# Performance work log

Hardware: AMD Instinct MI355X
Metric: run time of the kernel (lower is better)

The kernel has to match this reference:

```python
import jax, jax.numpy as jnp
import numpy as np

N, E = 50000, 800000
IN_DIM, HID, H1, H2, NCLS = 512, 64, 4, 1, 40
NEG_SLOPE = 0.2


def gat_conv(x, src, dst, W, att_src, att_dst, b, heads, ch):
    # x: [N, F_in]; W: [F_in, heads*ch]; att_*: [heads, ch]; b: [heads*ch]
    n = x.shape[0]
    h = (x @ W).reshape(n, heads, ch)                      # [N,H,C]
    a_s = jnp.einsum('nhc,hc->nh', h, att_src)             # [N,H]
    a_d = jnp.einsum('nhc,hc->nh', h, att_dst)             # [N,H]
    e = jax.nn.leaky_relu(a_s[src] + a_d[dst], NEG_SLOPE)  # [E,H]
    # segment softmax over incoming edges of each destination node
    m = jax.ops.segment_max(e, dst, num_segments=n)        # [N,H]
    ex = jnp.exp(e - m[dst])
    s = jax.ops.segment_sum(ex, dst, num_segments=n)       # [N,H]
    alpha = ex / (s[dst] + 1e-16)                          # [E,H]
    out = jax.ops.segment_sum(alpha[:, :, None] * h[src], dst, num_segments=n)
    return out.reshape(n, heads * ch) + b


def setup_inputs() -> dict:
    key = jax.random.key(0)
    ks = jax.random.split(key, 10)
    glorot = lambda k, shp: jax.random.normal(k, shp, jnp.float32) * jnp.sqrt(2.0 / (shp[0] + shp[-1]))
    return {
        'x': jax.random.normal(ks[0], (N, IN_DIM), jnp.float32),
        'edge_index': jax.random.randint(ks[1], (2, E), 0, N, jnp.int64),
        'W1': glorot(ks[2], (IN_DIM, H1 * HID)),
        'att_src1': glorot(ks[3], (H1, HID)),
        'att_dst1': glorot(ks[4], (H1, HID)),
        'b1': jnp.zeros((H1 * HID,), jnp.float32),
        'W2': glorot(ks[5], (H1 * HID, H2 * NCLS)),
        'att_src2': glorot(ks[6], (H2, NCLS)),
        'att_dst2': glorot(ks[7], (H2, NCLS)),
        'b2': jnp.zeros((H2 * NCLS,), jnp.float32),
    }


def reference(x, edge_index, W1, att_src1, att_dst1, b1, W2, att_src2, att_dst2, b2):
    n = x.shape[0]
    loops = jnp.arange(n, dtype=edge_index.dtype)
    src = jnp.concatenate([edge_index[0], loops])  # add self loops (PyG default)
    dst = jnp.concatenate([edge_index[1], loops])
    # dropout layers are identity in eval mode
    h = gat_conv(x, src, dst, W1, att_src1, att_dst1, b1, H1, HID)
    h = jax.nn.elu(h)
    out = gat_conv(h, src, dst, W2, att_src2, att_dst2, b2, H2, NCLS)
    return jax.nn.log_softmax(out, axis=1)
```

## Files before the change

### kernel.cpp

```cpp
#include <hip/hip_runtime.h>
#include <math.h>
#include <stdint.h>


typedef short bf16x8 __attribute__((ext_vector_type(8)));
typedef float f32x4  __attribute__((ext_vector_type(4)));

static __device__ __forceinline__ float leaky(float x){ return x > 0.f ? x : 0.2f*x; }
static __device__ __forceinline__ unsigned short f2bf(float f){
  uint32_t u = __float_as_uint(f);
  uint32_t r = u + 0x7fffu + ((u >> 16) & 1u);
  return (unsigned short)(r >> 16);
}
static __device__ __forceinline__ float bf2f(unsigned short u){
  return __uint_as_float(((uint32_t)u) << 16);
}

__global__ void k_cvt_x(const float* __restrict__ x, unsigned short* __restrict__ xb, int n4){
  int i = blockIdx.x*blockDim.x + threadIdx.x;
  if (i >= n4) return;
  float4 v = ((const float4*)x)[i];
  ushort4 o; o.x=f2bf(v.x); o.y=f2bf(v.y); o.z=f2bf(v.z); o.w=f2bf(v.w);
  ((ushort4*)xb)[i] = o;
}

__global__ void k_cvt_w(const float* __restrict__ W, unsigned short* __restrict__ wt){
  int i = blockIdx.x*blockDim.x + threadIdx.x;
  if (i >= 512*256) return;
  int k = i >> 8, n = i & 255;
  wt[n*512 + k] = f2bf(W[i]);
}

__global__ void k_count(const int* __restrict__ ei, int E, int n, int* __restrict__ deg){
  int i = blockIdx.x*blockDim.x + threadIdx.x;
  int tot = E + n;
  if (i >= tot) return;
  int dst = (i < E) ? ei[E + i] : (i - E);
  atomicAdd(&deg[dst], 1);
}

__global__ __launch_bounds__(256) void k_scan_a(const int* __restrict__ deg,
    int* __restrict__ rowstart, int* __restrict__ bsum, int n){
  __shared__ int sm[256];
  int b = blockIdx.x, t = threadIdx.x;
  int i = b*256 + t;
  int v = (i < n) ? deg[i] : 0;
  sm[t] = v;
  __syncthreads();
  for (int off=1; off<256; off<<=1){
    int u = (t >= off) ? sm[t-off] : 0;
    __syncthreads();
    sm[t] += u;
    __syncthreads();
  }
  if (i < n) rowstart[i+1] = sm[t];
  if (t == 255) bsum[b] = sm[255];
}
__global__ __launch_bounds__(256) void k_scan_b(int* __restrict__ bsum, int nb){
  __shared__ int sm[256];
  int t = threadIdx.x;
  int v = (t < nb) ? bsum[t] : 0;
  sm[t] = v;
  __syncthreads();
  for (int off=1; off<256; off<<=1){
    int u = (t >= off) ? sm[t-off] : 0;
    __syncthreads();
    sm[t] += u;
    __syncthreads();
  }
  if (t < nb) bsum[t] = sm[t] - v;
}
__global__ __launch_bounds__(256) void k_scan_c(int* __restrict__ rowstart,
    const int* __restrict__ bsum, int n){
  int b = blockIdx.x, t = threadIdx.x;
  int i = b*256 + t;
  if (i < n) rowstart[i+1] += bsum[b];
  if (i == 0) rowstart[0] = 0;
}

__global__ void k_fill(const int* __restrict__ ei, int E, int n,
                       const int* __restrict__ rowstart, int* __restrict__ cur, int* __restrict__ csr){
  int i = blockIdx.x*blockDim.x + threadIdx.x;
  int tot = E + n;
  if (i >= tot) return;
  int src, dst;
  if (i < E){ src = ei[i]; dst = ei[E+i]; } else { src = i - E; dst = src; }
  int pos = atomicAdd(&cur[dst], 1);
  csr[rowstart[dst] + pos] = src;
}

__global__ __launch_bounds__(256) void k_gemm1_mfma(const unsigned short* __restrict__ A,
                                                    const unsigned short* __restrict__ BT,
                                                    const float* __restrict__ SW,
                                                    const float* __restrict__ DW,
                                                    unsigned short* __restrict__ Cb,
                                                    float* __restrict__ as1,
                                                    float* __restrict__ ad1, int M){
  __shared__ __align__(16) unsigned short lA[4*128*8];
  __shared__ __align__(16) unsigned short lB[4*128*8];
  const int t = threadIdx.x;
  const int lane = t & 63, w = t >> 6;
  const int wx = w & 1, wy = w >> 1;
  const int row0 = blockIdx.x * 128, col0 = blockIdx.y * 128;

  f32x4 acc[4][4];
  #pragma unroll
  for (int i=0;i<4;i++)
    #pragma unroll
    for (int j=0;j<4;j++)
      #pragma unroll
      for (int r=0;r<4;r++) acc[i][j][r] = 0.f;

  const int c0 = t, c1 = t + 256;
  const int r0 = c0 & 127, kq0 = c0 >> 7;
  const int r1 = c1 & 127, kq1 = c1 >> 7;
  const size_t gA0 = (size_t)min(row0 + r0, M-1)*512 + kq0*8;
  const size_t gA1 = (size_t)min(row0 + r1, M-1)*512 + kq1*8;
  const size_t gB0 = (size_t)(col0 + r0)*512 + kq0*8;
  const size_t gB1 = (size_t)(col0 + r1)*512 + kq1*8;

  const int kq = lane >> 4, li = lane & 15;

  for (int kt = 0; kt < 512; kt += 32){
    __builtin_amdgcn_global_load_lds((const __attribute__((address_space(1))) void*)(A + gA0 + kt),
        (__attribute__((address_space(3))) void*)&lA[c0*8], 16, 0, 0);
    __builtin_amdgcn_global_load_lds((const __attribute__((address_space(1))) void*)(A + gA1 + kt),
        (__attribute__((address_space(3))) void*)&lA[c1*8], 16, 0, 0);
    __builtin_amdgcn_global_load_lds((const __attribute__((address_space(1))) void*)(BT + gB0 + kt),
        (__attribute__((address_space(3))) void*)&lB[c0*8], 16, 0, 0);
    __builtin_amdgcn_global_load_lds((const __attribute__((address_space(1))) void*)(BT + gB1 + kt),
        (__attribute__((address_space(3))) void*)&lB[c1*8], 16, 0, 0);
    __syncthreads();

    bf16x8 af[4], bfr[4];
    #pragma unroll
    for (int i=0;i<4;i++){
      af[i]  = *(const bf16x8*)&lA[(kq*128 + wx*64 + i*16 + li)*8];
      bfr[i] = *(const bf16x8*)&lB[(kq*128 + wy*64 + i*16 + li)*8];
    }
    #pragma unroll
    for (int i=0;i<4;i++)
      #pragma unroll
      for (int j=0;j<4;j++)
        acc[i][j] = __builtin_amdgcn_mfma_f32_16x16x32_bf16(af[i], bfr[j], acc[i][j], 0, 0, 0);
    __syncthreads();
  }

  #pragma unroll
  for (int i=0;i<4;i++){
    #pragma unroll
    for (int r=0;r<4;r++){
      int row = row0 + wx*64 + i*16 + kq*4 + r;
      if (row < M){
        #pragma unroll
        for (int j=0;j<4;j++)
          Cb[(size_t)row*256 + col0 + wy*64 + j*16 + li] = f2bf(acc[i][j][r]);
      }
    }
  }

  const int hw = (int)blockIdx.y*2 + wy;
  float sv[4], dv[4];
  #pragma unroll
  for (int j=0;j<4;j++){
    sv[j] = SW[hw*64 + j*16 + li];
    dv[j] = DW[hw*64 + j*16 + li];
  }
  #pragma unroll
  for (int i=0;i<4;i++){
    #pragma unroll
    for (int r=0;r<4;r++){
      float ps = acc[i][0][r]*sv[0] + acc[i][1][r]*sv[1] + acc[i][2][r]*sv[2] + acc[i][3][r]*sv[3];
      float pd = acc[i][0][r]*dv[0] + acc[i][1][r]*dv[1] + acc[i][2][r]*dv[2] + acc[i][3][r]*dv[3];
      #pragma unroll
      for (int o=1;o<16;o<<=1){ ps += __shfl_xor(ps,o); pd += __shfl_xor(pd,o); }
      int row = row0 + wx*64 + i*16 + kq*4 + r;
      if (li == 0 && row < M){
        as1[row*4 + hw] = ps;
        ad1[row*4 + hw] = pd;
      }
    }
  }
}

__global__ __launch_bounds__(256) void k_agg1(const unsigned short* __restrict__ h1b,
    const float* __restrict__ as1, const float* __restrict__ ad1,
    const int* __restrict__ rowstart, const int* __restrict__ csr,
    const float* __restrict__ b1, unsigned short* __restrict__ hactb, int n){
  int lane = threadIdx.x & 63;
  int node = blockIdx.x*4 + (threadIdx.x >> 6);
  if (node >= n) return;
  int lo = rowstart[node], hi = rowstart[node+1];
  int jj = lane >> 2, hh = lane & 3;
  float adh_p = ad1[node*4 + hh];

  float m = -INFINITY;
  for (int c = lo + jj; c < hi; c += 16){
    int s = csr[c];
    m = fmaxf(m, leaky(as1[s*4 + hh] + adh_p));
  }
  #pragma unroll
  for (int o=4;o<64;o<<=1) m = fmaxf(m, __shfl_xor(m,o));

  int h = lane >> 4;
  float ax=0.f, ay=0.f, az=0.f, aw=0.f, psum=0.f;
  for (int c = lo; c < hi; c += 16){
    int cnt = min(16, hi - c);
    int s_l = 0; float ex_l = 0.f;
    if (jj < cnt){
      s_l = csr[c + jj];
      ex_l = __expf(leaky(as1[s_l*4 + hh] + adh_p) - m);
    }
    psum += ex_l;
    int j = 0;
    for (; j + 3 < cnt; j += 4){
      int   s0 = __shfl(s_l, j*4),      s1 = __shfl(s_l, j*4+4),
            s2 = __shfl(s_l, j*4+8),    s3 = __shfl(s_l, j*4+12);
      float e0 = __shfl(ex_l, j*4+h),   e1 = __shfl(ex_l, j*4+4+h),
            e2 = __shfl(ex_l, j*4+8+h), e3 = __shfl(ex_l, j*4+12+h);
      ushort4 u0 = *(const ushort4*)(h1b + (size_t)s0*256 + lane*4);
      ushort4 u1 = *(const ushort4*)(h1b + (size_t)s1*256 + lane*4);
      ushort4 u2 = *(const ushort4*)(h1b + (size_t)s2*256 + lane*4);
      ushort4 u3 = *(const ushort4*)(h1b + (size_t)s3*256 + lane*4);
      ax += e0*bf2f(u0.x) + e1*bf2f(u1.x) + e2*bf2f(u2.x) + e3*bf2f(u3.x);
      ay += e0*bf2f(u0.y) + e1*bf2f(u1.y) + e2*bf2f(u2.y) + e3*bf2f(u3.y);
      az += e0*bf2f(u0.z) + e1*bf2f(u1.z) + e2*bf2f(u2.z) + e3*bf2f(u3.z);
      aw += e0*bf2f(u0.w) + e1*bf2f(u1.w) + e2*bf2f(u2.w) + e3*bf2f(u3.w);
    }
    for (; j < cnt; ++j){
      int   s0 = __shfl(s_l, j*4);
      float e0 = __shfl(ex_l, j*4+h);
      ushort4 u0 = *(const ushort4*)(h1b + (size_t)s0*256 + lane*4);
      ax += e0*bf2f(u0.x); ay += e0*bf2f(u0.y); az += e0*bf2f(u0.z); aw += e0*bf2f(u0.w);
    }
  }
  #pragma unroll
  for (int o=4;o<64;o<<=1) psum += __shfl_xor(psum,o);
  float ssum = __shfl(psum, h);
  float inv = 1.f/(ssum + 1e-16f);
  float4 bv = *(const float4*)(b1 + lane*4);
  float o0 = ax*inv + bv.x, o1 = ay*inv + bv.y, o2 = az*inv + bv.z, o3 = aw*inv + bv.w;
  ushort4 r;
  r.x = f2bf(o0 > 0.f ? o0 : expm1f(o0));
  r.y = f2bf(o1 > 0.f ? o1 : expm1f(o1));
  r.z = f2bf(o2 > 0.f ? o2 : expm1f(o2));
  r.w = f2bf(o3 > 0.f ? o3 : expm1f(o3));
  *(ushort4*)(hactb + (size_t)node*256 + lane*4) = r;
}

__global__ __launch_bounds__(256) void k_gemm2(const unsigned short* __restrict__ A,
    const float* __restrict__ B, const float* __restrict__ sw, const float* __restrict__ dw,
    unsigned short* __restrict__ Cb, float* __restrict__ as2, float* __restrict__ ad2, int M){
  __shared__ float Xl[32][129];
  __shared__ float Wl[128*40];
  __shared__ float Sps[32][8], Spd[32][8];
  int t = threadIdx.x;
  int row0 = blockIdx.x*32;
  int r = t & 31, g = t >> 5;
  float acc[5] = {0,0,0,0,0};
  for (int kt=0; kt<256; kt+=128){
    for (int i=t; i<1280; i+=256)
      *(float4*)&Wl[i*4] = *(const float4*)(B + kt*40 + i*4);
    for (int i=t; i<512; i+=256){
      int rr = i >> 4, k8 = i & 15;
      int grow = row0 + rr; if (grow >= M) grow = M-1;
      uint4 v = *(const uint4*)(A + (size_t)grow*256 + kt + k8*8);
      float* xp = &Xl[rr][k8*8];
      xp[0] = __uint_as_float(v.x << 16); xp[1] = __uint_as_float(v.x & 0xffff0000u);
      xp[2] = __uint_as_float(v.y << 16); xp[3] = __uint_as_float(v.y & 0xffff0000u);
      xp[4] = __uint_as_float(v.z << 16); xp[5] = __uint_as_float(v.z & 0xffff0000u);
      xp[6] = __uint_as_float(v.w << 16); xp[7] = __uint_as_float(v.w & 0xffff0000u);
    }
    __syncthreads();
    #pragma unroll 4
    for (int k=0;k<128;++k){
      float a = Xl[r][k];
      const float* wp = &Wl[k*40 + g*5];
      #pragma unroll
      for (int j=0;j<5;++j) acc[j] += a * wp[j];
    }
    __syncthreads();
  }
  int grow = row0 + r;
  float ps = 0.f, pd = 0.f;
  #pragma unroll
  for (int j=0;j<5;++j){
    ps += acc[j] * sw[g*5+j];
    pd += acc[j] * dw[g*5+j];
  }
  Sps[r][g] = ps; Spd[r][g] = pd;
  if (grow < M){
    #pragma unroll
    for (int j=0;j<5;++j) Cb[(size_t)grow*40 + g*5 + j] = f2bf(acc[j]);
  }
  __syncthreads();
  if (t < 32){
    float a = 0.f, b = 0.f;
    #pragma unroll
    for (int g2=0; g2<8; ++g2){ a += Sps[t][g2]; b += Spd[t][g2]; }
    int rw = row0 + t;
    if (rw < M){ as2[rw] = a; ad2[rw] = b; }
  }
}

__global__ __launch_bounds__(256) void k_agg2(const unsigned short* __restrict__ h2b,
    const float* __restrict__ as2, const float* __restrict__ ad2,
    const int* __restrict__ rowstart, const int* __restrict__ csr,
    const float* __restrict__ b2, float* __restrict__ out, int n){
  int lane = threadIdx.x & 63;
  int node = blockIdx.x*4 + (threadIdx.x >> 6);
  if (node >= n) return;
  int lo = rowstart[node], hi = rowstart[node+1];
  int deg = hi - lo;
  float adn = ad2[node];
  int   sl = 0;
  float ll = -INFINITY;
  if (lane < deg){ sl = csr[lo + lane]; ll = leaky(as2[sl] + adn); }
  float m = ll;
  for (int e = lo + lane + 64; e < hi; e += 64)
    m = fmaxf(m, leaky(as2[csr[e]] + adn));
  #pragma unroll
  for (int o=1;o<64;o<<=1) m = fmaxf(m, __shfl_xor(m,o));

  bool act = lane < 40;
  float acc = 0.f, psum = 0.f;
  for (int c = lo; c < hi; c += 64){
    int cnt = min(64, hi - c);
    int   s_l; float ex_l;
    if (c == lo){
      s_l = sl; ex_l = (lane < cnt) ? __expf(ll - m) : 0.f;
    } else {
      s_l = 0; ex_l = 0.f;
      if (lane < cnt){ s_l = csr[c + lane]; ex_l = __expf(leaky(as2[s_l] + adn) - m); }
    }
    psum += ex_l;
    int j = 0;
    for (; j + 3 < cnt; j += 4){
      int   s0=__shfl(s_l,j),  s1=__shfl(s_l,j+1),  s2=__shfl(s_l,j+2),  s3=__shfl(s_l,j+3);
      float e0=__shfl(ex_l,j), e1=__shfl(ex_l,j+1), e2=__shfl(ex_l,j+2), e3=__shfl(ex_l,j+3);
      float h0 = act ? bf2f(h2b[(size_t)s0*40 + lane]) : 0.f;
      float h1 = act ? bf2f(h2b[(size_t)s1*40 + lane]) : 0.f;
      float h2 = act ? bf2f(h2b[(size_t)s2*40 + lane]) : 0.f;
      float h3 = act ? bf2f(h2b[(size_t)s3*40 + lane]) : 0.f;
      acc += e0*h0; acc += e1*h1; acc += e2*h2; acc += e3*h3;
    }
    for (; j < cnt; ++j){
      int s0=__shfl(s_l,j); float e0=__shfl(ex_l,j);
      acc += e0 * (act ? bf2f(h2b[(size_t)s0*40 + lane]) : 0.f);
    }
  }
  float ssum = psum;
  #pragma unroll
  for (int o=1;o<64;o<<=1) ssum += __shfl_xor(ssum,o);
  float ov = acc/(ssum + 1e-16f) + (act ? b2[lane] : 0.f);
  float v = act ? ov : -INFINITY;
  float mx = v;
  #pragma unroll
  for (int o=1;o<64;o<<=1) mx = fmaxf(mx, __shfl_xor(mx,o));
  float ev = act ? __expf(ov - mx) : 0.f;
  float se = ev;
  #pragma unroll
  for (int o=1;o<64;o<<=1) se += __shfl_xor(se,o);
  if (act) out[(size_t)node*40 + lane] = (ov - mx) - __logf(se);
}

extern "C" void kernel_launch(void* const* d_in, const int* in_sizes, int n_in,
                              void* d_out, int out_size, void* d_ws, size_t ws_size,
                              hipStream_t stream){
  const float* x   = (const float*)d_in[0];
  const int*   ei  = (const int*)d_in[1];
  const float* W1  = (const float*)d_in[2];
  const float* s1w = (const float*)d_in[3];
  const float* d1w = (const float*)d_in[4];
  const float* b1  = (const float*)d_in[5];
  const float* W2  = (const float*)d_in[6];
  const float* s2w = (const float*)d_in[7];
  const float* d2w = (const float*)d_in[8];
  const float* b2  = (const float*)d_in[9];
  float* out = (float*)d_out;

  const int N  = in_sizes[0] / 512;
  const int E  = in_sizes[1] / 2;
  const int Et = E + N;

  float* f = (float*)d_ws;
  unsigned short* h1b   = (unsigned short*)f;  f += (size_t)N*128;
  unsigned short* hactb = (unsigned short*)f;  f += (size_t)N*128;
  float* as1  = f;  f += (size_t)N*4;
  float* ad1  = f;  f += (size_t)N*4;
  float* as2  = f;  f += N;
  float* ad2  = f;  f += N;
  unsigned short* w1t = (unsigned short*)f;  f += 256*512/2;
  unsigned short* xb  = (unsigned short*)f;  f += (size_t)N*256;
  unsigned short* h2b = xb;
  int* ip = (int*)f;
  int* rowstart = ip;  ip += (N + 4) & ~3;
  int* deg      = ip;  ip += N;
  int* cur      = ip;  ip += N;
  int* csr      = ip;  ip += Et;
  int* bsum     = ip;  ip += 256;

  int nb4 = (N + 3) / 4;
  int n4  = (N*512)/4;
  int nbs = (N + 255) / 256;
  k_cvt_x<<<(n4+255)/256, 256, 0, stream>>>(x, xb, n4);
  k_cvt_w<<<512, 256, 0, stream>>>(W1, w1t);
  hipMemsetAsync(deg, 0, (size_t)2*N*sizeof(int), stream);
  k_count<<<(Et+255)/256, 256, 0, stream>>>(ei, E, N, deg);
  k_scan_a<<<nbs, 256, 0, stream>>>(deg, rowstart, bsum, N);
  k_scan_b<<<1, 256, 0, stream>>>(bsum, nbs);
  k_scan_c<<<nbs, 256, 0, stream>>>(rowstart, bsum, N);
  k_fill <<<(Et+255)/256, 256, 0, stream>>>(ei, E, N, rowstart, cur, csr);
  k_gemm1_mfma<<<dim3((N+127)/128, 2), 256, 0, stream>>>(xb, w1t, s1w, d1w, h1b, as1, ad1, N);
  k_agg1 <<<nb4, 256, 0, stream>>>(h1b, as1, ad1, rowstart, csr, b1, hactb, N);
  k_gemm2<<<(N+31)/32, 256, 0, stream>>>(hactb, W2, s2w, d2w, h2b, as2, ad2, N);
  k_agg2 <<<nb4, 256, 0, stream>>>(h2b, as2, ad2, rowstart, csr, b2, out, N);
}
```

Before: 474.2 us.

## Split edge softmax into separate precompute kernels and drop memset launch

Moves the per-edge attention max/exp/sum computation out of both aggregation kernels into new k_pre1/k_pre2 kernels. These write per-edge exp weights and per-node inverse sums into scratch carved from the bf16 x buffer. The aggregation kernels then loop over edges with wave-uniform indices instead of shuffling weights across lanes. The deg/cur zeroing memset is folded into existing kernels to remove a launch. This adds two kernel launches and extra global traffic for the exp buffers, and relies on the scratch offsets inside xb not overlapping h2b or live data.

After: 500.4 us. 5.5% more time.

```diff
diff --git a/kernel.cpp b/kernel.cpp
--- a/kernel.cpp
+++ b/kernel.cpp
@@ -24,11 +24,13 @@
   ((ushort4*)xb)[i] = o;
 }
 
-__global__ void k_cvt_w(const float* __restrict__ W, unsigned short* __restrict__ wt){
+__global__ void k_cvt_w(const float* __restrict__ W, unsigned short* __restrict__ wt,
+                        int* __restrict__ deg, int n){
   int i = blockIdx.x*blockDim.x + threadIdx.x;
+  if (i < n) deg[i] = 0;
   if (i >= 512*256) return;
-  int k = i >> 8, n = i & 255;
-  wt[n*512 + k] = f2bf(W[i]);
+  int k = i >> 8, c = i & 255;
+  wt[c*512 + k] = f2bf(W[i]);
 }
 
 __global__ void k_count(const int* __restrict__ ei, int E, int n, int* __restrict__ deg){
@@ -71,10 +73,10 @@
   if (t < nb) bsum[t] = sm[t] - v;
 }
 __global__ __launch_bounds__(256) void k_scan_c(int* __restrict__ rowstart,
-    const int* __restrict__ bsum, int n){
+    const int* __restrict__ bsum, int* __restrict__ cur, int n){
   int b = blockIdx.x, t = threadIdx.x;
   int i = b*256 + t;
-  if (i < n) rowstart[i+1] += bsum[b];
+  if (i < n){ rowstart[i+1] += bsum[b]; cur[i] = 0; }
   if (i == 0) rowstart[0] = 0;
 }
 
@@ -183,61 +185,64 @@
   }
 }
 
+__global__ __launch_bounds__(256) void k_pre1(const float* __restrict__ as1,
+    const float* __restrict__ ad1, const int* __restrict__ rowstart,
+    const int* __restrict__ csr, float* __restrict__ exbuf, float* __restrict__ inv1, int n){
+  int lane = threadIdx.x & 63;
+  int node = blockIdx.x*4 + (threadIdx.x >> 6);
+  if (node >= n) return;
+  int lo = rowstart[node], hi = rowstart[node+1];
+  int jj = lane >> 2, hh = lane & 3;
+  float adh = ad1[node*4 + hh];
+  float m = -INFINITY;
+  for (int c = lo + jj; c < hi; c += 16)
+    m = fmaxf(m, leaky(as1[csr[c]*4 + hh] + adh));
+  #pragma unroll
+  for (int o=4;o<64;o<<=1) m = fmaxf(m, __shfl_xor(m,o));
+  float psum = 0.f;
+  for (int c = lo + jj; c < hi; c += 16){
+    float ex = __expf(leaky(as1[csr[c]*4 + hh] + adh) - m);
+    exbuf[(size_t)c*4 + hh] = ex;
+    psum += ex;
+  }
+  #pragma unroll
+  for (int o=4;o<64;o<<=1) psum += __shfl_xor(psum,o);
+  if (jj == 0) inv1[node*4 + hh] = 1.f/(psum + 1e-16f);
+}
+
 __global__ __launch_bounds__(256) void k_agg1(const unsigned short* __restrict__ h1b,
-    const float* __restrict__ as1, const float* __restrict__ ad1,
+    const float* __restrict__ exbuf, const float* __restrict__ inv1,
     const int* __restrict__ rowstart, const int* __restrict__ csr,
     const float* __restrict__ b1, unsigned short* __restrict__ hactb, int n){
   int lane = threadIdx.x & 63;
   int node = blockIdx.x*4 + (threadIdx.x >> 6);
   if (node >= n) return;
-  int lo = rowstart[node], hi = rowstart[node+1];
-  int jj = lane >> 2, hh = lane & 3;
-  float adh_p = ad1[node*4 + hh];
-
-  float m = -INFINITY;
-  for (int c = lo + jj; c < hi; c += 16){
-    int s = csr[c];
-    m = fmaxf(m, leaky(as1[s*4 + hh] + adh_p));
-  }
-  #pragma unroll
-  for (int o=4;o<64;o<<=1) m = fmaxf(m, __shfl_xor(m,o));
-
+  int lo = __builtin_amdgcn_readfirstlane(rowstart[node]);
+  int hi = __builtin_amdgcn_readfirstlane(rowstart[node+1]);
   int h = lane >> 4;
-  float ax=0.f, ay=0.f, az=0.f, aw=0.f, psum=0.f;
-  for (int c = lo; c < hi; c += 16){
-    int cnt = min(16, hi - c);
-    int s_l = 0; float ex_l = 0.f;
-    if (jj < cnt){
-      s_l = csr[c + jj];
-      ex_l = __expf(leaky(as1[s_l*4 + hh] + adh_p) - m);
-    }
-    psum += ex_l;
-    int j = 0;
-    for (; j + 3 < cnt; j += 4){
-      int   s0 = __shfl(s_l, j*4),      s1 = __shfl(s_l, j*4+4),
-            s2 = __shfl(s_l, j*4+8),    s3 = __shfl(s_l, j*4+12);
-      float e0 = __shfl(ex_l, j*4+h),   e1 = __shfl(ex_l, j*4+4+h),
-            e2 = __shfl(ex_l, j*4+8+h), e3 = __shfl(ex_l, j*4+12+h);
-      ushort4 u0 = *(const ushort4*)(h1b + (size_t)s0*256 + lane*4);
-      ushort4 u1 = *(const ushort4*)(h1b + (size_t)s1*256 + lane*4);
-      ushort4 u2 = *(const ushort4*)(h1b + (size_t)s2*256 + lane*4);
-      ushort4 u3 = *(const ushort4*)(h1b + (size_t)s3*256 + lane*4);
-      ax += e0*bf2f(u0.x) + e1*bf2f(u1.x) + e2*bf2f(u2.x) + e3*bf2f(u3.x);
-      ay += e0*bf2f(u0.y) + e1*bf2f(u1.y) + e2*bf2f(u2.y) + e3*bf2f(u3.y);
-      az += e0*bf2f(u0.z) + e1*bf2f(u1.z) + e2*bf2f(u2.z) + e3*bf2f(u3.z);
-      aw += e0*bf2f(u0.w) + e1*bf2f(u1.w) + e2*bf2f(u2.w) + e3*bf2f(u3.w);
-    }
-    for (; j < cnt; ++j){
-      int   s0 = __shfl(s_l, j*4);
-      float e0 = __shfl(ex_l, j*4+h);
-      ushort4 u0 = *(const ushort4*)(h1b + (size_t)s0*256 + lane*4);
-      ax += e0*bf2f(u0.x); ay += e0*bf2f(u0.y); az += e0*bf2f(u0.z); aw += e0*bf2f(u0.w);
-    }
-  }
-  #pragma unroll
-  for (int o=4;o<64;o<<=1) psum += __shfl_xor(psum,o);
-  float ssum = __shfl(psum, h);
-  float inv = 1.f/(ssum + 1e-16f);
+  const float* exb = exbuf + h;
+  float ax=0.f, ay=0.f, az=0.f, aw=0.f;
+  int e = lo;
+  for (; e + 3 < hi; e += 4){
+    int s0 = csr[e], s1 = csr[e+1], s2 = csr[e+2], s3 = csr[e+3];
+    float e0 = exb[(size_t)e*4],     e1 = exb[(size_t)(e+1)*4],
+          e2 = exb[(size_t)(e+2)*4], e3 = exb[(size_t)(e+3)*4];
+    ushort4 u0 = *(const ushort4*)(h1b + (size_t)s0*256 + lane*4);
+    ushort4 u1 = *(const ushort4*)(h1b + (size_t)s1*256 + lane*4);
+    ushort4 u2 = *(const ushort4*)(h1b + (size_t)s2*256 + lane*4);
+    ushort4 u3 = *(const ushort4*)(h1b + (size_t)s3*256 + lane*4);
+    ax += e0*bf2f(u0.x) + e1*bf2f(u1.x) + e2*bf2f(u2.x) + e3*bf2f(u3.x);
+    ay += e0*bf2f(u0.y) + e1*bf2f(u1.y) + e2*bf2f(u2.y) + e3*bf2f(u3.y);
+    az += e0*bf2f(u0.z) + e1*bf2f(u1.z) + e2*bf2f(u2.z) + e3*bf2f(u3.z);
+    aw += e0*bf2f(u0.w) + e1*bf2f(u1.w) + e2*bf2f(u2.w) + e3*bf2f(u3.w);
+  }
+  for (; e < hi; ++e){
+    int s0 = csr[e];
+    float e0 = exb[(size_t)e*4];
+    ushort4 u0 = *(const ushort4*)(h1b + (size_t)s0*256 + lane*4);
+    ax += e0*bf2f(u0.x); ay += e0*bf2f(u0.y); az += e0*bf2f(u0.z); aw += e0*bf2f(u0.w);
+  }
+  float inv = inv1[node*4 + h];
   float4 bv = *(const float4*)(b1 + lane*4);
   float o0 = ax*inv + bv.x, o1 = ay*inv + bv.y, o2 = az*inv + bv.z, o3 = aw*inv + bv.w;
   ushort4 r;
@@ -303,56 +308,56 @@
   }
 }
 
+__global__ __launch_bounds__(256) void k_pre2(const float* __restrict__ as2,
+    const float* __restrict__ ad2, const int* __restrict__ rowstart,
+    const int* __restrict__ csr, float* __restrict__ ex2, float* __restrict__ inv2, int n){
+  int lane = threadIdx.x & 63;
+  int node = blockIdx.x*4 + (threadIdx.x >> 6);
+  if (node >= n) return;
+  int lo = rowstart[node], hi = rowstart[node+1];
+  float adn = ad2[node];
+  float m = -INFINITY;
+  for (int e = lo + lane; e < hi; e += 64)
+    m = fmaxf(m, leaky(as2[csr[e]] + adn));
+  #pragma unroll
+  for (int o=1;o<64;o<<=1) m = fmaxf(m, __shfl_xor(m,o));
+  float psum = 0.f;
+  for (int e = lo + lane; e < hi; e += 64){
+    float ex = __expf(leaky(as2[csr[e]] + adn) - m);
+    ex2[e] = ex;
+    psum += ex;
+  }
+  #pragma unroll
+  for (int o=1;o<64;o<<=1) psum += __shfl_xor(psum,o);
+  if (lane == 0) inv2[node] = 1.f/(psum + 1e-16f);
+}
+
 __global__ __launch_bounds__(256) void k_agg2(const unsigned short* __restrict__ h2b,
-    const float* __restrict__ as2, const float* __restrict__ ad2,
+    const float* __restrict__ ex2, const float* __restrict__ inv2,
     const int* __restrict__ rowstart, const int* __restrict__ csr,
     const float* __restrict__ b2, float* __restrict__ out, int n){
   int lane = threadIdx.x & 63;
   int node = blockIdx.x*4 + (threadIdx.x >> 6);
   if (node >= n) return;
-  int lo = rowstart[node], hi = rowstart[node+1];
-  int deg = hi - lo;
-  float adn = ad2[node];
-  int   sl = 0;
-  float ll = -INFINITY;
-  if (lane < deg){ sl = csr[lo + lane]; ll = leaky(as2[sl] + adn); }
-  float m = ll;
-  for (int e = lo + lane + 64; e < hi; e += 64)
-    m = fmaxf(m, leaky(as2[csr[e]] + adn));
-  #pragma unroll
-  for (int o=1;o<64;o<<=1) m = fmaxf(m, __shfl_xor(m,o));
-
+  int lo = __builtin_amdgcn_readfirstlane(rowstart[node]);
+  int hi = __builtin_amdgcn_readfirstlane(rowstart[node+1]);
   bool act = lane < 40;
-  float acc = 0.f, psum = 0.f;
-  for (int c = lo; c < hi; c += 64){
-    int cnt = min(64, hi - c);
-    int   s_l; float ex_l;
-    if (c == lo){
-      s_l = sl; ex_l = (lane < cnt) ? __expf(ll - m) : 0.f;
-    } else {
-      s_l = 0; ex_l = 0.f;
-      if (lane < cnt){ s_l = csr[c + lane]; ex_l = __expf(leaky(as2[s_l] + adn) - m); }
-    }
-    psum += ex_l;
-    int j = 0;
-    for (; j + 3 < cnt; j += 4){
-      int   s0=__shfl(s_l,j),  s1=__shfl(s_l,j+1),  s2=__shfl(s_l,j+2),  s3=__shfl(s_l,j+3);
-      float e0=__shfl(ex_l,j), e1=__shfl(ex_l,j+1), e2=__shfl(ex_l,j+2), e3=__shfl(ex_l,j+3);
-      float h0 = act ? bf2f(h2b[(size_t)s0*40 + lane]) : 0.f;
-      float h1 = act ? bf2f(h2b[(size_t)s1*40 + lane]) : 0.f;
-      float h2 = act ? bf2f(h2b[(size_t)s2*40 + lane]) : 0.f;
-      float h3 = act ? bf2f(h2b[(size_t)s3*40 + lane]) : 0.f;
-      acc += e0*h0; acc += e1*h1; acc += e2*h2; acc += e3*h3;
-    }
-    for (; j < cnt; ++j){
-      int s0=__shfl(s_l,j); float e0=__shfl(ex_l,j);
-      acc += e0 * (act ? bf2f(h2b[(size_t)s0*40 + lane]) : 0.f);
-    }
-  }
-  float ssum = psum;
-  #pragma unroll
-  for (int o=1;o<64;o<<=1) ssum += __shfl_xor(ssum,o);
-  float ov = acc/(ssum + 1e-16f) + (act ? b2[lane] : 0.f);
+  float acc = 0.f;
+  int e = lo;
+  for (; e + 3 < hi; e += 4){
+    int s0 = csr[e], s1 = csr[e+1], s2 = csr[e+2], s3 = csr[e+3];
+    float e0 = ex2[e], e1 = ex2[e+1], e2 = ex2[e+2], e3 = ex2[e+3];
+    float h0 = act ? bf2f(h2b[(size_t)s0*40 + lane]) : 0.f;
+    float h1 = act ? bf2f(h2b[(size_t)s1*40 + lane]) : 0.f;
+    float h2 = act ? bf2f(h2b[(size_t)s2*40 + lane]) : 0.f;
+    float h3 = act ? bf2f(h2b[(size_t)s3*40 + lane]) : 0.f;
+    acc += e0*h0 + e1*h1 + e2*h2 + e3*h3;
+  }
+  for (; e < hi; ++e){
+    int s0 = csr[e]; float e0 = ex2[e];
+    acc += e0 * (act ? bf2f(h2b[(size_t)s0*40 + lane]) : 0.f);
+  }
+  float ov = acc*inv2[node] + (act ? b2[lane] : 0.f);
   float v = act ? ov : -INFINITY;
   float mx = v;
   #pragma unroll
@@ -390,9 +395,13 @@
   float* ad1  = f;  f += (size_t)N*4;
   float* as2  = f;  f += N;
   float* ad2  = f;  f += N;
+  float* inv1 = f;  f += (size_t)N*4;
+  float* inv2 = f;  f += N;
   unsigned short* w1t = (unsigned short*)f;  f += 256*512/2;
   unsigned short* xb  = (unsigned short*)f;  f += (size_t)N*256;
-  unsigned short* h2b = xb;
+  unsigned short* h2b   = xb;
+  float*          exbuf = (float*)(xb + (size_t)4*1024*1024);
+  float*          ex2   = (float*)(xb + (size_t)12*1024*1024);
   int* ip = (int*)f;
   int* rowstart = ip;  ip += (N + 4) & ~3;
   int* deg      = ip;  ip += N;
@@ -404,15 +413,16 @@
   int n4  = (N*512)/4;
   int nbs = (N + 255) / 256;
   k_cvt_x<<<(n4+255)/256, 256, 0, stream>>>(x, xb, n4);
-  k_cvt_w<<<512, 256, 0, stream>>>(W1, w1t);
-  hipMemsetAsync(deg, 0, (size_t)2*N*sizeof(int), stream);
+  k_cvt_w<<<512, 256, 0, stream>>>(W1, w1t, deg, N);
   k_count<<<(Et+255)/256, 256, 0, stream>>>(ei, E, N, deg);
   k_scan_a<<<nbs, 256, 0, stream>>>(deg, rowstart, bsum, N);
   k_scan_b<<<1, 256, 0, stream>>>(bsum, nbs);
-  k_scan_c<<<nbs, 256, 0, stream>>>(rowstart, bsum, N);
+  k_scan_c<<<nbs, 256, 0, stream>>>(rowstart, bsum, cur, N);
   k_fill <<<(Et+255)/256, 256, 0, stream>>>(ei, E, N, rowstart, cur, csr);
   k_gemm1_mfma<<<dim3((N+127)/128, 2), 256, 0, stream>>>(xb, w1t, s1w, d1w, h1b, as1, ad1, N);
-  k_agg1 <<<nb4, 256, 0, stream>>>(h1b, as1, ad1, rowstart, csr, b1, hactb, N);
+  k_pre1 <<<nb4, 256, 0, stream>>>(as1, ad1, rowstart, csr, exbuf, inv1, N);
+  k_agg1 <<<nb4, 256, 0, stream>>>(h1b, exbuf, inv1, rowstart, csr, b1, hactb, N);
   k_gemm2<<<(N+31)/32, 256, 0, stream>>>(hactb, W2, s2w, d2w, h2b, as2, ad2, N);
-  k_agg2 <<<nb4, 256, 0, stream>>>(h2b, as2, ad2, rowstart, csr, b2, out, N);
-}
+  k_pre2 <<<nb4, 256, 0, stream>>>(as2, ad2, rowstart, csr, ex2, inv2, N);
+  k_agg2 <<<nb4, 256, 0, stream>>>(h2b, ex2, inv2, rowstart, csr, b2, out, N);
+}
```
